# Kernel optimization log

Measured on AMD Instinct MI355X. Metric: run time of the kernel, lower is better.

## Reference

```python
import jax, jax.numpy as jnp
import numpy as np

B, L, G, F = 64, 2048, 512, 3072
N = L + G + F            # nodes per graph
NT = B * N               # total flattened nodes
EG = 16384               # edges per graph (shared topology)
E = B * EG
H, D_IN, NUM_LAYERS = 64, 7, 4
EPS = 1e-5


def setup_inputs() -> dict:
    key = jax.random.key(0)
    ks = jax.random.split(key, 8)
    rng = np.random.default_rng(0)
    x = jax.random.normal(ks[0], (NT, D_IN), jnp.float32)
    # shared topology, replicated per graph with node offsets (PyG batched graph)
    eg = rng.integers(0, N, size=(2, EG))
    offs = (np.arange(B) * N)[None, :, None]
    edge_index = jnp.asarray((eg[:, None, :] + offs).reshape(2, E), dtype=jnp.int32)
    base = np.arange(B)[:, None] * N  # per-graph layout: [loc | gen | line]
    loc_idx = jnp.asarray((base + np.arange(0, L)[None, :]).reshape(-1), jnp.int32)
    prod_idx = jnp.asarray((base + np.arange(L, L + G)[None, :]).reshape(-1), jnp.int32)
    line_idx = jnp.asarray((base + np.arange(L + G, N)[None, :]).reshape(-1), jnp.int32)
    # gen->loc incidence [L, G]: each generator sits at one location
    gm = np.zeros((L, G), np.float32)
    gm[rng.integers(0, L, G), np.arange(G)] = 1.0
    # line->loc signed incidence [L, F]: +1 at from-bus, -1 at to-bus
    lm = np.zeros((L, F), np.float32)
    lm[rng.integers(0, L, F), np.arange(F)] += 1.0
    lm[rng.integers(0, L, F), np.arange(F)] -= 1.0
    s = 1.0 / np.sqrt(H)
    se = 1.0 / np.sqrt(D_IN)
    enc_w = jax.random.uniform(ks[1], (H, D_IN), jnp.float32, -se, se)
    enc_b = jnp.zeros((H,), jnp.float32)
    w_rel = jax.random.uniform(ks[2], (NUM_LAYERS, H, H), jnp.float32, -s, s)
    b_rel = jnp.zeros((NUM_LAYERS, H), jnp.float32)
    w_root = jax.random.uniform(ks[3], (NUM_LAYERS, H, H), jnp.float32, -s, s)
    ln_g = jnp.ones((H,), jnp.float32)
    ln_b = jnp.zeros((H,), jnp.float32)
    prod_w = jax.random.uniform(ks[4], (1, H), jnp.float32, -s, s)
    prod_b = jnp.zeros((1,), jnp.float32)
    flow_w = jax.random.uniform(ks[5], (1, H), jnp.float32, -s, s)
    flow_b = jnp.zeros((1,), jnp.float32)
    return {"x": x, "edge_index": edge_index, "prod_idx": prod_idx,
            "line_idx": line_idx, "loc_idx": loc_idx, "enc_w": enc_w, "enc_b": enc_b,
            "ln_g": ln_g, "ln_b": ln_b, "w_rel": w_rel, "b_rel": b_rel, "w_root": w_root,
            "prod_w": prod_w, "prod_b": prod_b, "flow_w": flow_w, "flow_b": flow_b,
            "gen_mask": jnp.asarray(gm), "line_mask": jnp.asarray(lm)}


def reference(x, edge_index, prod_idx, line_idx, loc_idx, enc_w, enc_b, ln_g, ln_b,
              w_rel, b_rel, w_root, prod_w, prod_b, flow_w, flow_b, gen_mask, line_mask):
    h = jax.nn.relu(x @ enc_w.T + enc_b)                       # [NT, H]
    src, dst = edge_index[0], edge_index[1]
    for i in range(NUM_LAYERS):
        # LayerNorm (shared across layers, as in the torch module)
        mu = jnp.mean(h, axis=-1, keepdims=True)
        var = jnp.mean((h - mu) ** 2, axis=-1, keepdims=True)
        hn = (h - mu) * jax.lax.rsqrt(var + EPS) * ln_g + ln_b
        # GraphConv: W_rel * sum_{j in N(i)} h_j + b_rel + W_root * h_i
        agg = jax.ops.segment_sum(hn[src], dst, num_segments=NT)  # gather + scatter-add
        h = jax.nn.relu(agg @ w_rel[i].T + b_rel[i] + hn @ w_root[i].T)
    p = (h[prod_idx] @ prod_w.T + prod_b).reshape(B, G)
    f = (h[line_idx] @ flow_w.T + flow_b).reshape(B, F)
    demand = x[loc_idx, 0].reshape(B, L)
    md = demand - (p @ gen_mask.T + f @ line_mask.T)           # unmet demand [B, L]
    return (p, f, md)
```

## Files before the change

### kernel.cpp

```cpp
#include <hip/hip_runtime.h>

#define B_ 64
#define L_ 2048
#define G_ 512
#define F_ 3072
#define N_ 5632
#define NT_ 360448
#define EG_ 16384
#define E_ 1048576
#define EPS_ 1e-5f
#define KTOT_ 3584
#define KCH_ 448
#define TCAP_ 384

typedef __attribute__((ext_vector_type(8))) short bf8v;
typedef __attribute__((ext_vector_type(4))) float f4v;

__device__ __forceinline__ unsigned short f2bf(float f){
  unsigned int u=__float_as_uint(f);
  unsigned int r=(u + 0x7fffu + ((u>>16)&1u))>>16;
  return (unsigned short)r;
}
__device__ __forceinline__ float bf2f(unsigned short h){
  return __uint_as_float(((unsigned int)h)<<16);
}

__global__ __launch_bounds__(256) void k_prep(const int* __restrict__ ei,
    unsigned short* __restrict__ wcat,
    const float* __restrict__ wrel, const float* __restrict__ wroot,
    int* __restrict__ offT, int* __restrict__ srcs2,
    const float* __restrict__ x, const int* __restrict__ loci, float* __restrict__ outmd,
    unsigned short* __restrict__ hn, const float* __restrict__ ew, const float* __restrict__ eb,
    const float* __restrict__ lng, const float* __restrict__ lnb){
  int bid=blockIdx.x, tid=threadIdx.x;
  if(bid>=600){
    int lane=tid&63, wid=tid>>6;
    int idx=bid-600;
    int gid=idx/88;
    int nb0=(idx%88)*64 + wid*16;
    int ng=lane>>4;
    int lig=lane&15;
    float w[4][7], bias[4], gam[4], bet[4];
    #pragma unroll
    for(int j=0;j<4;j++){
      int c=lig*4+j;
      #pragma unroll
      for(int k=0;k<7;k++) w[j][k]=ew[c*7+k];
      bias[j]=eb[c]; gam[j]=lng[c]; bet[j]=lnb[c];
    }
    #pragma unroll
    for(int t=0;t<4;t++){
      int n=nb0 + t*4 + ng;
      long xrow=((long)gid*N_+n)*7;
      float xv[7];
      #pragma unroll
      for(int k=0;k<7;k++) xv[k]=x[xrow+k];
      float h[4]; float s1=0.f, s2=0.f;
      #pragma unroll
      for(int j=0;j<4;j++){
        float a=bias[j];
        #pragma unroll
        for(int k=0;k<7;k++) a+=xv[k]*w[j][k];
        a=fmaxf(a,0.f);
        h[j]=a; s1+=a; s2+=a*a;
      }
      #pragma unroll
      for(int o=1;o<16;o<<=1){ s1+=__shfl_xor(s1,o,64); s2+=__shfl_xor(s2,o,64); }
      float mu=s1*(1.f/64.f);
      float var=s2*(1.f/64.f)-mu*mu;
      float inv=rsqrtf(var+EPS_);
      unsigned int p0=(unsigned int)f2bf((h[0]-mu)*inv*gam[0]+bet[0])
                    | ((unsigned int)f2bf((h[1]-mu)*inv*gam[1]+bet[1])<<16);
      unsigned int p1=(unsigned int)f2bf((h[2]-mu)*inv*gam[2]+bet[2])
                    | ((unsigned int)f2bf((h[3]-mu)*inv*gam[3]+bet[3])<<16);
      *(uint2*)(hn + (size_t)n*4096 + gid*64 + lig*4) = (uint2){p0,p1};
    }
    return;
  }
  if(bid>=88){
    int i=(bid-88)*256+tid;
    if(i<B_*L_) outmd[i]=x[(long)loci[i]*7];
    if(i<32768){
      int l=i>>13; int rest=i&8191; int n=rest>>7; int k=rest&127;
      float v=(k<64)? wrel[((long)l*64+n)*64+k] : wroot[((long)l*64+n)*64+(k-64)];
      wcat[i]=f2bf(v);
    }
    return;
  }
  __shared__ int cnt64[64], cur64[64];
  int nb=bid*64;
  if(tid<64) cnt64[tid]=0;
  __syncthreads();
  for(int e=tid;e<EG_;e+=256){
    int d=ei[E_+e];
    unsigned t=(unsigned)(d-nb);
    if(t<64u) atomicAdd(&cnt64[t],1);
  }
  __syncthreads();
  if(tid<64){
    int v=cnt64[tid], s=v;
    #pragma unroll
    for(int o=1;o<64;o<<=1){ int u=__shfl_up(s,o,64); if(tid>=o) s+=u; }
    int ex=s-v;
    offT[bid*65+tid]=ex;
    cur64[tid]=ex;
    if(tid==63) offT[bid*65+64]=s;
  }
  __syncthreads();
  for(int e=tid;e<EG_;e+=256){
    int s=ei[e];
    int d=ei[E_+e];
    unsigned t=(unsigned)(d-nb);
    if(t<64u){
      int p=atomicAdd(&cur64[t],1);
      if(p<TCAP_) srcs2[bid*TCAP_+p]=s|(d<<16);
    }
  }
}

__device__ __forceinline__ void upadd(float* a, uint4 qa, uint4 qb){
  unsigned int t[8]={qa.x,qa.y,qa.z,qa.w,qb.x,qb.y,qb.z,qb.w};
  #pragma unroll
  for(int j=0;j<8;j++){
    a[2*j]   += __uint_as_float(t[j]<<16);
    a[2*j+1] += __uint_as_float(t[j]&0xffff0000u);
  }
}

__device__ __forceinline__ void stw16(char* base, int r, int chunk, unsigned int p0,
                                      unsigned int p1, unsigned int p2, unsigned int p3){
  int byte = r*128 + chunk*16;
  byte ^= (r&7)<<4;
  *(uint4*)(base + byte) = (uint4){p0,p1,p2,p3};
}
__device__ __forceinline__ bf8v ld16(const char* base, int r, int chunk){
  int byte = r*128 + chunk*16;
  byte ^= (r&7)<<4;
  return *(const bf8v*)(base + byte);
}

__global__ __launch_bounds__(256,6) void k_layer(const unsigned short* __restrict__ hs,
    unsigned short* __restrict__ hd, const int* __restrict__ offT, const int* __restrict__ srcs2,
    const unsigned short* __restrict__ wcat, const float* __restrict__ brel,
    const float* __restrict__ lng, const float* __restrict__ lnb, int do_ln){
  __shared__ uint4 aggl4[1024];
  char* agglc=(char*)aggl4;
  int tid=threadIdx.x;
  int w=tid>>6, lane=tid&63;
  int dst0=blockIdx.x*2;

  {
    int jj=dst0>>6, loc=dst0&63;
    int kb=offT[jj*65+loc];
    int ke=offT[jj*65+loc+2];
    const int* esp=srcs2 + jj*TCAP_;
    int co=tid*16;
    float aA[16], aB[16];
    #pragma unroll
    for(int c=0;c<16;c++){ aA[c]=0.f; aB[c]=0.f; }
    for(int k=kb;k<ke;k+=4){
      int nrem=ke-k;
      int i1=(nrem>1)?k+1:k;
      int i2=(nrem>2)?k+2:k;
      int i3=(nrem>3)?k+3:k;
      int u0=esp[k], u1=esp[i1], u2=esp[i2], u3=esp[i3];
      const unsigned short* r0=hs+(size_t)(u0&0xffff)*4096+co;
      const unsigned short* r1=hs+(size_t)(u1&0xffff)*4096+co;
      const unsigned short* r2=hs+(size_t)(u2&0xffff)*4096+co;
      const unsigned short* r3=hs+(size_t)(u3&0xffff)*4096+co;
      uint4 qa0=*(const uint4*)r0, qb0=*(const uint4*)(r0+8);
      uint4 qa1=*(const uint4*)r1, qb1=*(const uint4*)(r1+8);
      uint4 qa2=*(const uint4*)r2, qb2=*(const uint4*)(r2+8);
      uint4 qa3=*(const uint4*)r3, qb3=*(const uint4*)(r3+8);
      if((u0>>16)==dst0) upadd(aA,qa0,qb0); else upadd(aB,qa0,qb0);
      if(nrem>1){ if((u1>>16)==dst0) upadd(aA,qa1,qb1); else upadd(aB,qa1,qb1); }
      if(nrem>2){ if((u2>>16)==dst0) upadd(aA,qa2,qb2); else upadd(aB,qa2,qb2); }
      if(nrem>3){ if((u3>>16)==dst0) upadd(aA,qa3,qb3); else upadd(aB,qa3,qb3); }
    }
    unsigned int pA[8], pB[8];
    #pragma unroll
    for(int j=0;j<8;j++){
      pA[j]=(unsigned int)f2bf(aA[2*j]) | ((unsigned int)f2bf(aA[2*j+1])<<16);
      pB[j]=(unsigned int)f2bf(aB[2*j]) | ((unsigned int)f2bf(aB[2*j+1])<<16);
    }
    int rl=tid>>2, c2=(tid&3)*2;
    stw16(agglc, rl,    c2,   pA[0],pA[1],pA[2],pA[3]);
    stw16(agglc, rl,    c2+1, pA[4],pA[5],pA[6],pA[7]);
    stw16(agglc, 64+rl, c2,   pB[0],pB[1],pB[2],pB[3]);
    stw16(agglc, 64+rl, c2+1, pB[4],pB[5],pB[6],pB[7]);
  }
  __syncthreads();

  int m=lane&15, quad=lane>>4;
  f4v acc[2][4];
  float bias_nt[4], g_nt[4], b_nt[4];
  #pragma unroll
  for(int nt=0;nt<4;nt++){
    int c=nt*16+m;
    bias_nt[nt]=brel[c];
    g_nt[nt]=lng[c]; b_nt[nt]=lnb[c];
    acc[0][nt]=(f4v){0.f,0.f,0.f,0.f};
    acc[1][nt]=(f4v){0.f,0.f,0.f,0.f};
  }
  #pragma unroll
  for(int mt=0;mt<2;mt++){
    int R=w*32+mt*16+m;
    bf8v af0=ld16(agglc,R,quad);
    bf8v af1=ld16(agglc,R,4+quad);
    int dn=dst0+(R>>6), gg=R&63;
    const unsigned short* hrow=hs+(size_t)dn*4096+gg*64;
    bf8v af2=*(const bf8v*)(hrow+quad*8);
    bf8v af3=*(const bf8v*)(hrow+32+quad*8);
    #pragma unroll
    for(int nt=0;nt<4;nt++){
      const unsigned short* wrow=wcat + (long)(nt*16+m)*128 + quad*8;
      bf8v b0=*(const bf8v*)(wrow);
      bf8v b1=*(const bf8v*)(wrow+32);
      bf8v b2=*(const bf8v*)(wrow+64);
      bf8v b3=*(const bf8v*)(wrow+96);
      acc[mt][nt]=__builtin_amdgcn_mfma_f32_16x16x32_bf16(af0,b0,acc[mt][nt],0,0,0);
      acc[mt][nt]=__builtin_amdgcn_mfma_f32_16x16x32_bf16(af1,b1,acc[mt][nt],0,0,0);
      acc[mt][nt]=__builtin_amdgcn_mfma_f32_16x16x32_bf16(af2,b2,acc[mt][nt],0,0,0);
      acc[mt][nt]=__builtin_amdgcn_mfma_f32_16x16x32_bf16(af3,b3,acc[mt][nt],0,0,0);
    }
  }
  #pragma unroll
  for(int mt=0;mt<2;mt++){
    float v[4][4];
    #pragma unroll
    for(int nt=0;nt<4;nt++)
      #pragma unroll
      for(int r=0;r<4;r++)
        v[nt][r]=fmaxf(acc[mt][nt][r]+bias_nt[nt],0.f);
    if(do_ln){
      #pragma unroll
      for(int r=0;r<4;r++){
        float rs=v[0][r]+v[1][r]+v[2][r]+v[3][r];
        float rss=v[0][r]*v[0][r]+v[1][r]*v[1][r]+v[2][r]*v[2][r]+v[3][r]*v[3][r];
        #pragma unroll
        for(int o=1;o<16;o<<=1){ rs+=__shfl_xor(rs,o,64); rss+=__shfl_xor(rss,o,64); }
        float mu=rs*(1.f/64.f);
        float var=rss*(1.f/64.f)-mu*mu;
        float inv=rsqrtf(var+EPS_);
        #pragma unroll
        for(int nt=0;nt<4;nt++) v[nt][r]=(v[nt][r]-mu)*inv*g_nt[nt]+b_nt[nt];
      }
    }
    #pragma unroll
    for(int r=0;r<4;r++){
      int R=w*32+mt*16+quad*4+r;
      int dn=dst0+(R>>6), gg=R&63;
      unsigned short* out=hd + (size_t)dn*4096 + gg*64;
      #pragma unroll
      for(int nt=0;nt<4;nt++) out[nt*16+m]=f2bf(v[nt][r]);
    }
  }
}

__global__ __launch_bounds__(256) void k_readout2(const unsigned short* __restrict__ h,
    const int* __restrict__ prodi, const int* __restrict__ linei,
    const float* __restrict__ pw, const float* __restrict__ pb,
    const float* __restrict__ fw, const float* __restrict__ fb,
    float* __restrict__ outp, float* __restrict__ outf,
    unsigned short* __restrict__ pfhi, unsigned short* __restrict__ pflo){
  int i=blockIdx.x*256+threadIdx.x;
  const int MP=B_*G_;
  const int MT=MP+B_*F_;
  if(i>=MT) return;
  bool isp=i<MP;
  int j=isp? i : i-MP;
  unsigned nf=(unsigned)(isp? prodi[j] : linei[j]);
  unsigned gg=nf/(unsigned)N_;
  unsigned node=nf-gg*(unsigned)N_;
  const float* wv=isp? pw:fw;
  float acc=isp? pb[0]:fb[0];
  const uint4* hp=(const uint4*)(h + (size_t)node*4096 + gg*64);
  #pragma unroll
  for(int c=0;c<8;c++){
    uint4 u=hp[c];
    unsigned int uu[4]={u.x,u.y,u.z,u.w};
    #pragma unroll
    for(int q=0;q<4;q++){
      float lo=__uint_as_float(uu[q]<<16);
      float hi=__uint_as_float(uu[q]&0xffff0000u);
      acc += lo*wv[c*8+2*q] + hi*wv[c*8+2*q+1];
    }
  }
  int b,kcol;
  if(isp){ outp[j]=acc; b=j/G_; kcol=j%G_; }
  else   { outf[j]=acc; b=j/F_; kcol=G_+j%F_; }
  unsigned short hi=f2bf(acc);
  pfhi[(long)b*KTOT_+kcol]=hi;
  pflo[(long)b*KTOT_+kcol]=f2bf(acc-bf2f(hi));
}

__global__ __launch_bounds__(256) void k_md_gemm(const float* __restrict__ gm, const float* __restrict__ lm,
    const unsigned short* __restrict__ pfhi, const unsigned short* __restrict__ pflo,
    float* __restrict__ outmd){
  int tid=threadIdx.x;
  int w=tid>>6, lane=tid&63;
  int m=lane&15, quad=lane>>4;
  int lb=blockIdx.x>>3, kc=blockIdx.x&7;
  int l=lb*64 + w*16 + m;
  f4v acc[4];
  #pragma unroll
  for(int nt=0;nt<4;nt++) acc[nt]=(f4v){0.f,0.f,0.f,0.f};
  int kk0=kc*KCH_;
  for(int s=0;s<KCH_/32;s++){
    int kk=kk0+s*32;
    const float* ap = (kk<G_)? gm + (long)l*G_ + kk : lm + (long)l*F_ + (kk-G_);
    float4 a0=*(const float4*)(ap+quad*8);
    float4 a1=*(const float4*)(ap+quad*8+4);
    bf8v af;
    af[0]=(short)f2bf(a0.x); af[1]=(short)f2bf(a0.y);
    af[2]=(short)f2bf(a0.z); af[3]=(short)f2bf(a0.w);
    af[4]=(short)f2bf(a1.x); af[5]=(short)f2bf(a1.y);
    af[6]=(short)f2bf(a1.z); af[7]=(short)f2bf(a1.w);
    #pragma unroll
    for(int nt=0;nt<4;nt++){
      int b=nt*16+m;
      const unsigned short* bp=pfhi + (long)b*KTOT_ + kk + quad*8;
      const unsigned short* lp=pflo + (long)b*KTOT_ + kk + quad*8;
      bf8v bh=*(const bf8v*)bp;
      bf8v bl=*(const bf8v*)lp;
      acc[nt]=__builtin_amdgcn_mfma_f32_16x16x32_bf16(af,bh,acc[nt],0,0,0);
      acc[nt]=__builtin_amdgcn_mfma_f32_16x16x32_bf16(af,bl,acc[nt],0,0,0);
    }
  }
  int lrow=lb*64 + w*16 + quad*4;
  #pragma unroll
  for(int r=0;r<4;r++)
    #pragma unroll
    for(int nt=0;nt<4;nt++)
      atomicAdd(&outmd[(long)(nt*16+m)*L_ + lrow+r], -acc[nt][r]);
}

extern "C" void kernel_launch(void* const* d_in, const int* in_sizes, int n_in,
                              void* d_out, int out_size, void* d_ws, size_t ws_size,
                              hipStream_t stream){
  const float* x    =(const float*)d_in[0];
  const int*   ei   =(const int*)d_in[1];
  const int*   prodi=(const int*)d_in[2];
  const int*   linei=(const int*)d_in[3];
  const int*   loci =(const int*)d_in[4];
  const float* ew   =(const float*)d_in[5];
  const float* eb   =(const float*)d_in[6];
  const float* lng  =(const float*)d_in[7];
  const float* lnb  =(const float*)d_in[8];
  const float* wrel =(const float*)d_in[9];
  const float* brel =(const float*)d_in[10];
  const float* wroot=(const float*)d_in[11];
  const float* pw   =(const float*)d_in[12];
  const float* pb   =(const float*)d_in[13];
  const float* fw   =(const float*)d_in[14];
  const float* fb   =(const float*)d_in[15];
  const float* gm   =(const float*)d_in[16];
  const float* lm   =(const float*)d_in[17];

  char* ws=(char*)d_ws;
  unsigned short* hnA =(unsigned short*)ws;
  unsigned short* hnB =hnA + (size_t)NT_*64;
  unsigned short* wcat=hnB + (size_t)NT_*64;
  unsigned short* pfhi=wcat + 32768;
  unsigned short* pflo=pfhi + (size_t)B_*KTOT_;
  int* offT =(int*)(pflo + (size_t)B_*KTOT_);
  int* srcs2=offT + 88*65;

  float* outp =(float*)d_out;
  float* outf =outp + (size_t)B_*G_;
  float* outmd=outf + (size_t)B_*F_;

  k_prep<<<600+NT_/64,256,0,stream>>>(ei,wcat,wrel,wroot,offT,srcs2,
                                      x,loci,outmd,hnA,ew,eb,lng,lnb);
  for(int i=0;i<4;i++){
    const unsigned short* hs=(i&1)?hnB:hnA;
    unsigned short* hd=(i&1)?hnA:hnB;
    k_layer<<<N_/2,256,0,stream>>>(hs,hd,offT,srcs2,wcat+(size_t)i*8192,
        brel+(size_t)i*64,lng,lnb,(i<3)?1:0);
  }
  {
    int MT=B_*(G_+F_);
    k_readout2<<<(MT+255)/256,256,0,stream>>>(hnA,prodi,linei,pw,pb,fw,fb,outp,outf,pfhi,pflo);
  }
  k_md_gemm<<<256,256,0,stream>>>(gm,lm,pfhi,pflo,outmd);
}
```

Baseline: 435.0 us.

## Retile GraphConv layer kernel to 32 nodes by 4 graphs with XCD-aware block mapping

Each layer block now covers 32 node ids across a 4-graph chunk (256 columns) instead of 2 node ids across all 64 graphs. Each wavefront owns 8 destination nodes and keeps per-node register accumulators selected by a switch. Edge indices are made wave-uniform with readfirstlane, and the block-to-tile mapping is arranged so each XCD works on its own set of graph chunks, with the aim of better L2 locality for gathered rows. Output is staged through LDS so global stores are coalesced 16-byte writes. The costs are more edge-list rereads across chunks, higher register pressure (occupancy hint lowered to 5), and an extra barrier.

```diff
diff --git a/kernel.cpp b/kernel.cpp
--- a/kernel.cpp
+++ b/kernel.cpp
@@ -118,20 +118,10 @@
   }
 }
 
-__device__ __forceinline__ void upadd(float* a, uint4 qa, uint4 qb){
-  unsigned int t[8]={qa.x,qa.y,qa.z,qa.w,qb.x,qb.y,qb.z,qb.w};
-  #pragma unroll
-  for(int j=0;j<8;j++){
-    a[2*j]   += __uint_as_float(t[j]<<16);
-    a[2*j+1] += __uint_as_float(t[j]&0xffff0000u);
-  }
-}
-
-__device__ __forceinline__ void stw16(char* base, int r, int chunk, unsigned int p0,
-                                      unsigned int p1, unsigned int p2, unsigned int p3){
-  int byte = r*128 + chunk*16;
+__device__ __forceinline__ void stw8(char* base, int r, int c8, unsigned int p0, unsigned int p1){
+  int byte = r*128 + c8*8;
   byte ^= (r&7)<<4;
-  *(uint4*)(base + byte) = (uint4){p0,p1,p2,p3};
+  *(uint2*)(base + byte) = (uint2){p0,p1};
 }
 __device__ __forceinline__ bf8v ld16(const char* base, int r, int chunk){
   int byte = r*128 + chunk*16;
@@ -139,7 +129,20 @@
   return *(const bf8v*)(base + byte);
 }
 
-__global__ __launch_bounds__(256,6) void k_layer(const unsigned short* __restrict__ hs,
+#define ADDE_(u,qv) { int d_=((u)>>16)-n0;                                        \
+  float l0_=__uint_as_float((qv).x<<16), h0_=__uint_as_float((qv).x&0xffff0000u); \
+  float l1_=__uint_as_float((qv).y<<16), h1_=__uint_as_float((qv).y&0xffff0000u); \
+  switch(d_){                                                                     \
+    case 0: acc[0][0]+=l0_;acc[0][1]+=h0_;acc[0][2]+=l1_;acc[0][3]+=h1_; break;   \
+    case 1: acc[1][0]+=l0_;acc[1][1]+=h0_;acc[1][2]+=l1_;acc[1][3]+=h1_; break;   \
+    case 2: acc[2][0]+=l0_;acc[2][1]+=h0_;acc[2][2]+=l1_;acc[2][3]+=h1_; break;   \
+    case 3: acc[3][0]+=l0_;acc[3][1]+=h0_;acc[3][2]+=l1_;acc[3][3]+=h1_; break;   \
+    case 4: acc[4][0]+=l0_;acc[4][1]+=h0_;acc[4][2]+=l1_;acc[4][3]+=h1_; break;   \
+    case 5: acc[5][0]+=l0_;acc[5][1]+=h0_;acc[5][2]+=l1_;acc[5][3]+=h1_; break;   \
+    case 6: acc[6][0]+=l0_;acc[6][1]+=h0_;acc[6][2]+=l1_;acc[6][3]+=h1_; break;   \
+    default:acc[7][0]+=l0_;acc[7][1]+=h0_;acc[7][2]+=l1_;acc[7][3]+=h1_; break; } }
+
+__global__ __launch_bounds__(256,5) void k_layer(const unsigned short* __restrict__ hs,
     unsigned short* __restrict__ hd, const int* __restrict__ offT, const int* __restrict__ srcs2,
     const unsigned short* __restrict__ wcat, const float* __restrict__ brel,
     const float* __restrict__ lng, const float* __restrict__ lnb, int do_ln){
@@ -147,47 +150,50 @@
   char* agglc=(char*)aggl4;
   int tid=threadIdx.x;
   int w=tid>>6, lane=tid&63;
-  int dst0=blockIdx.x*2;
+  int bid=blockIdx.x;
+  int xcd=bid&7, bq=bid>>3;
+  int chunk=xcd + 8*(bq/176);
+  int tile =bq%176;
+  int n0t=tile*32;
+  int cb=chunk*256;
 
   {
-    int jj=dst0>>6, loc=dst0&63;
-    int kb=offT[jj*65+loc];
-    int ke=offT[jj*65+loc+2];
+    int n0=n0t+w*8;
+    int jj=n0>>6, loc=n0&63;
+    int kb=__builtin_amdgcn_readfirstlane(offT[jj*65+loc]);
+    int ke=__builtin_amdgcn_readfirstlane(offT[jj*65+loc+8]);
     const int* esp=srcs2 + jj*TCAP_;
-    int co=tid*16;
-    float aA[16], aB[16];
-    #pragma unroll
-    for(int c=0;c<16;c++){ aA[c]=0.f; aB[c]=0.f; }
+    int cw=cb + lane*4;
+    float acc[8][4];
+    #pragma unroll
+    for(int j=0;j<8;j++){ acc[j][0]=0.f;acc[j][1]=0.f;acc[j][2]=0.f;acc[j][3]=0.f; }
     for(int k=kb;k<ke;k+=4){
       int nrem=ke-k;
-      int i1=(nrem>1)?k+1:k;
-      int i2=(nrem>2)?k+2:k;
-      int i3=(nrem>3)?k+3:k;
-      int u0=esp[k], u1=esp[i1], u2=esp[i2], u3=esp[i3];
-      const unsigned short* r0=hs+(size_t)(u0&0xffff)*4096+co;
-      const unsigned short* r1=hs+(size_t)(u1&0xffff)*4096+co;
-      const unsigned short* r2=hs+(size_t)(u2&0xffff)*4096+co;
-      const unsigned short* r3=hs+(size_t)(u3&0xffff)*4096+co;
-      uint4 qa0=*(const uint4*)r0, qb0=*(const uint4*)(r0+8);
-      uint4 qa1=*(const uint4*)r1, qb1=*(const uint4*)(r1+8);
-      uint4 qa2=*(const uint4*)r2, qb2=*(const uint4*)(r2+8);
-      uint4 qa3=*(const uint4*)r3, qb3=*(const uint4*)(r3+8);
-      if((u0>>16)==dst0) upadd(aA,qa0,qb0); else upadd(aB,qa0,qb0);
-      if(nrem>1){ if((u1>>16)==dst0) upadd(aA,qa1,qb1); else upadd(aB,qa1,qb1); }
-      if(nrem>2){ if((u2>>16)==dst0) upadd(aA,qa2,qb2); else upadd(aB,qa2,qb2); }
-      if(nrem>3){ if((u3>>16)==dst0) upadd(aA,qa3,qb3); else upadd(aB,qa3,qb3); }
-    }
-    unsigned int pA[8], pB[8];
+      int u0=__builtin_amdgcn_readfirstlane(esp[k]);
+      int u1=__builtin_amdgcn_readfirstlane(esp[(nrem>1)?k+1:k]);
+      int u2=__builtin_amdgcn_readfirstlane(esp[(nrem>2)?k+2:k]);
+      int u3=__builtin_amdgcn_readfirstlane(esp[(nrem>3)?k+3:k]);
+      const unsigned short* r0=hs+(size_t)(u0&0xffff)*4096+cw;
+      const unsigned short* r1=hs+(size_t)(u1&0xffff)*4096+cw;
+      const unsigned short* r2=hs+(size_t)(u2&0xffff)*4096+cw;
+      const unsigned short* r3=hs+(size_t)(u3&0xffff)*4096+cw;
+      uint2 e0=*(const uint2*)r0;
+      uint2 e1=*(const uint2*)r1;
+      uint2 e2=*(const uint2*)r2;
+      uint2 e3=*(const uint2*)r3;
+      ADDE_(u0,e0);
+      if(nrem>1) ADDE_(u1,e1);
+      if(nrem>2) ADDE_(u2,e2);
+      if(nrem>3) ADDE_(u3,e3);
+    }
+    int g=lane>>4, c8=lane&15;
     #pragma unroll
     for(int j=0;j<8;j++){
-      pA[j]=(unsigned int)f2bf(aA[2*j]) | ((unsigned int)f2bf(aA[2*j+1])<<16);
-      pB[j]=(unsigned int)f2bf(aB[2*j]) | ((unsigned int)f2bf(aB[2*j+1])<<16);
-    }
-    int rl=tid>>2, c2=(tid&3)*2;
-    stw16(agglc, rl,    c2,   pA[0],pA[1],pA[2],pA[3]);
-    stw16(agglc, rl,    c2+1, pA[4],pA[5],pA[6],pA[7]);
-    stw16(agglc, 64+rl, c2,   pB[0],pB[1],pB[2],pB[3]);
-    stw16(agglc, 64+rl, c2+1, pB[4],pB[5],pB[6],pB[7]);
+      int R=(w*8+j)*4+g;
+      unsigned int p0=(unsigned int)f2bf(acc[j][0]) | ((unsigned int)f2bf(acc[j][1])<<16);
+      unsigned int p1=(unsigned int)f2bf(acc[j][2]) | ((unsigned int)f2bf(acc[j][3])<<16);
+      stw8(agglc,R,c8,p0,p1);
+    }
   }
   __syncthreads();
 
@@ -207,8 +213,8 @@
     int R=w*32+mt*16+m;
     bf8v af0=ld16(agglc,R,quad);
     bf8v af1=ld16(agglc,R,4+quad);
-    int dn=dst0+(R>>6), gg=R&63;
-    const unsigned short* hrow=hs+(size_t)dn*4096+gg*64;
+    int dn=n0t+(R>>2), gg=R&3;
+    const unsigned short* hrow=hs+(size_t)dn*4096+cb+gg*64;
     bf8v af2=*(const bf8v*)(hrow+quad*8);
     bf8v af3=*(const bf8v*)(hrow+32+quad*8);
     #pragma unroll
@@ -224,6 +230,9 @@
       acc[mt][nt]=__builtin_amdgcn_mfma_f32_16x16x32_bf16(af3,b3,acc[mt][nt],0,0,0);
     }
   }
+  __syncthreads();
+  unsigned short* ot=(unsigned short*)agglc;
+
   #pragma unroll
   for(int mt=0;mt<2;mt++){
     float v[4][4];
@@ -249,10 +258,20 @@
     #pragma unroll
     for(int r=0;r<4;r++){
       int R=w*32+mt*16+quad*4+r;
-      int dn=dst0+(R>>6), gg=R&63;
-      unsigned short* out=hd + (size_t)dn*4096 + gg*64;
-      #pragma unroll
-      for(int nt=0;nt<4;nt++) out[nt*16+m]=f2bf(v[nt][r]);
+      #pragma unroll
+      for(int nt=0;nt<4;nt++) ot[R*64 + nt*16+m]=f2bf(v[nt][r]);
+    }
+  }
+  __syncthreads();
+
+  {
+    int segoff=(tid&31)*8;
+    int nd0=tid>>5;
+    #pragma unroll
+    for(int nn=0;nn<4;nn++){
+      int node=nd0+nn*8;
+      uint4 val=*(const uint4*)(ot + node*256 + segoff);
+      *(uint4*)(hd + (size_t)(n0t+node)*4096 + cb + segoff) = val;
     }
   }
 }
@@ -375,7 +394,7 @@
   for(int i=0;i<4;i++){
     const unsigned short* hs=(i&1)?hnB:hnA;
     unsigned short* hd=(i&1)?hnA:hnB;
-    k_layer<<<N_/2,256,0,stream>>>(hs,hd,offT,srcs2,wcat+(size_t)i*8192,
+    k_layer<<<16*176,256,0,stream>>>(hs,hd,offT,srcs2,wcat+(size_t)i*8192,
         brel+(size_t)i*64,lng,lnb,(i<3)?1:0);
   }
   {
```

New measurement: 462.7 us. +6.4%, slower.
